# Performance work log

Hardware: AMD Instinct MI355X
Metric: run time of the kernel (lower is better)

Reference implementation:

```python
import jax, jax.numpy as jnp
import numpy as np

D_MODEL = 1024
D_STATE = 512
SEQ_LEN = 16384
R_MIN, R_MAX, MAX_PHASE = 0.0, 1.0, 6.28


def setup_inputs() -> dict:
    key = jax.random.key(0)
    ks = jax.random.split(key, 8)
    inputs = jax.random.normal(ks[0], (SEQ_LEN, D_MODEL), dtype=jnp.float32)
    # parameter init exactly as in the module
    u_nu = jax.random.uniform(ks[1], (D_STATE,), dtype=jnp.float32)
    nu_log = jnp.log(-0.5 * jnp.log(u_nu * (R_MAX ** 2 - R_MIN ** 2) + R_MIN ** 2))
    u_th = jax.random.uniform(ks[2], (D_STATE,), dtype=jnp.float32)
    theta_log = jnp.log(MAX_PHASE * u_th)
    diag_lambda = jnp.exp(-jnp.exp(nu_log) + 1j * jnp.exp(theta_log))
    gamma_log = jnp.log(jnp.sqrt(1.0 - jnp.abs(diag_lambda) ** 2))
    bn = jnp.sqrt(jnp.asarray(2 * D_MODEL, jnp.float32))
    cn = jnp.sqrt(jnp.asarray(D_STATE, jnp.float32))
    B_re = jax.random.normal(ks[3], (D_STATE, D_MODEL), dtype=jnp.float32) / bn
    B_im = jax.random.normal(ks[4], (D_STATE, D_MODEL), dtype=jnp.float32) / bn
    C_re = jax.random.normal(ks[5], (D_MODEL, D_STATE), dtype=jnp.float32) / cn
    C_im = jax.random.normal(ks[6], (D_MODEL, D_STATE), dtype=jnp.float32) / cn
    D = jax.random.normal(ks[7], (D_MODEL,), dtype=jnp.float32)
    return {"inputs": inputs, "nu_log": nu_log, "theta_log": theta_log,
            "gamma_log": gamma_log, "B_re": B_re, "B_im": B_im,
            "C_re": C_re, "C_im": C_im, "D": D}


def _binop(q_i, q_j):
    # associative combine for diagonal linear recurrence h' = a*h + b
    a_i, b_i = q_i
    a_j, b_j = q_j
    return (a_j * a_i, a_j * b_i + b_j)


def reference(inputs, nu_log, theta_log, gamma_log, B_re, B_im, C_re, C_im, D):
    L = inputs.shape[0]
    diag_lambda = jnp.exp(-jnp.exp(nu_log) + 1j * jnp.exp(theta_log))  # (d_state,)
    B_norm = (B_re + 1j * B_im) * jnp.exp(gamma_log)[:, None]          # (d_state, d_model)
    C = C_re + 1j * C_im                                               # (d_model, d_state)
    # Bu[t] = B_norm @ x_t  -> (L, d_state) complex
    Bu = inputs.astype(B_norm.dtype) @ B_norm.T
    Lambda_elems = jnp.broadcast_to(diag_lambda, (L, diag_lambda.shape[0]))
    _, h = jax.lax.associative_scan(_binop, (Lambda_elems, Bu))        # (L, d_state)
    # y_t = Re[C h_t] + D * x_t
    return jnp.real(h @ C.T) + D * inputs
```

## Files before the change

### kernel.cpp

```cpp
#include <hip/hip_runtime.h>
#include <math.h>

#define L_SEQ   16384
#define DMODEL  1024
#define NST     512
#define CHUNK   128
#define NCHUNK  (L_SEQ / CHUNK)

typedef float  f32x4 __attribute__((ext_vector_type(4)));
typedef short  s16x8 __attribute__((ext_vector_type(8)));

__device__ __forceinline__ unsigned short f2bf(float f) {
    union { float f; unsigned int u; } v; v.f = f;
    unsigned int r = v.u + 0x7fffu + ((v.u >> 16) & 1u);
    return (unsigned short)(r >> 16);
}
__device__ __forceinline__ unsigned short f2bf_fast(float f) {
    union { float f; unsigned int u; } v; v.f = f;
    return (unsigned short)((v.u + 0x8000u) >> 16);
}
__device__ __forceinline__ float bf2f(unsigned int h16) {
    union { unsigned int u; float f; } v; v.u = h16 << 16; return v.f;
}
__device__ __forceinline__ void mfma16(f32x4& d, s16x8 a, s16x8 b) {
    asm volatile("v_mfma_f32_16x16x32_bf16 %0, %1, %2, %0"
                 : "+v"(d) : "v"(a), "v"(b));
}
__device__ __forceinline__ uint4 pack8(float4 x, float4 y) {
    union { unsigned short u[8]; uint4 v; } t;
    t.u[0] = f2bf_fast(x.x); t.u[1] = f2bf_fast(x.y);
    t.u[2] = f2bf_fast(x.z); t.u[3] = f2bf_fast(x.w);
    t.u[4] = f2bf_fast(y.x); t.u[5] = f2bf_fast(y.y);
    t.u[6] = f2bf_fast(y.z); t.u[7] = f2bf_fast(y.w);
    return t.v;
}
__device__ __forceinline__ void gload16(const unsigned short* g, unsigned short* l) {
    __builtin_amdgcn_global_load_lds(
        (const __attribute__((address_space(1))) unsigned int*)g,
        (__attribute__((address_space(3))) unsigned int*)l,
        16, 0, 0);
}

__global__ void setup_params(const float* __restrict__ nu_log,
                             const float* __restrict__ theta_log,
                             const float* __restrict__ gamma_log,
                             float* __restrict__ lam,
                             float* __restrict__ lamT,
                             float* __restrict__ gam) {
    int s = threadIdx.x;
    if (s >= NST) return;
    float mod = expf(-expf(nu_log[s]));
    float th  = expf(theta_log[s]);
    float ar = mod * cosf(th);
    float ai = mod * sinf(th);
    lam[s] = ar; lam[NST + s] = ai;
    gam[s] = expf(gamma_log[s]);
    float pr = 1.f, pi = 0.f;
    for (int i = 0; i < CHUNK; ++i) {
        float nr = pr * ar - pi * ai;
        float ni = pr * ai + pi * ar;
        pr = nr; pi = ni;
    }
    lamT[s] = pr; lamT[NST + s] = pi;
}

__global__ void pack_w1(const float* __restrict__ Bre, const float* __restrict__ Bim,
                        unsigned short* __restrict__ W1) {
    int idx = blockIdx.x * 256 + threadIdx.x;
    int n = idx >> 10, k = idx & 1023;
    int s = n >> 1;
    float v = (n & 1) ? Bim[s * DMODEL + k] : Bre[s * DMODEL + k];
    W1[idx] = f2bf(v);
}
__global__ void pack_w2(const float* __restrict__ Cre, const float* __restrict__ Cim,
                        unsigned short* __restrict__ W2) {
    int idx = blockIdx.x * 256 + threadIdx.x;
    int n = idx >> 10, k = idx & 1023;
    int s = k >> 1;
    float v = (k & 1) ? -Cim[n * NST + s] : Cre[n * NST + s];
    W2[idx] = f2bf(v);
}

__global__ __launch_bounds__(256)
void conv_x(const float4* __restrict__ X, uint4* __restrict__ Xb) {
    int i = blockIdx.x * 256 + threadIdx.x;
    float4 a = X[2 * i], b = X[2 * i + 1];
    Xb[i] = pack8(a, b);
}

template<int EPI>
__global__ __launch_bounds__(256, 4)
void gemm_bf16(const unsigned short* __restrict__ A, const unsigned short* __restrict__ B,
               void* __restrict__ out, const float* __restrict__ Dv,
               const float* __restrict__ Xf) {
    const int K = 1024, N = 1024;
    __shared__ __align__(16) unsigned short As[128 * 64];
    __shared__ __align__(16) unsigned short Bs[128 * 64];

    const int tid  = threadIdx.x;
    const int lane = tid & 63;
    const int wave = tid >> 6;
    const int wr   = wave >> 1, wc = wave & 1;
    const int fr   = lane & 15;
    const int g4   = lane >> 4;
    const int f7   = fr & 7;

    const int lin   = blockIdx.y * gridDim.x + blockIdx.x;
    const int n_new = (lin & 7) * 128 + (lin >> 3);
    const int bx = n_new & 7, by = n_new >> 3;
    const int m0 = by * 128, n0 = bx * 128;

    const int srow   = tid >> 3;
    const int schunk = (tid & 7) ^ (srow & 7);
    const unsigned short* Asrc = A + (size_t)(m0 + srow) * K + schunk * 8;
    const unsigned short* Bsrc = B + (size_t)(n0 + srow) * K + schunk * 8;

    f32x4 acc[4][4] = {};

    for (int k0 = 0; k0 < K; k0 += 64) {
        __syncthreads();
        #pragma unroll
        for (int ld = 0; ld < 4; ++ld) {
            gload16(Asrc + (size_t)(ld * 32) * K + k0, &As[ld * 2048 + tid * 8]);
            gload16(Bsrc + (size_t)(ld * 32) * K + k0, &Bs[ld * 2048 + tid * 8]);
        }
        __syncthreads();

        #pragma unroll
        for (int h = 0; h < 2; ++h) {
            s16x8 af[4], bfq[4];
            #pragma unroll
            for (int i = 0; i < 4; ++i) {
                const int row = wr * 64 + i * 16 + fr;
                af[i] = *(const s16x8*)&As[row * 64 + (((h * 4 + g4) ^ f7) << 3)];
            }
            #pragma unroll
            for (int j = 0; j < 4; ++j) {
                const int row = wc * 64 + j * 16 + fr;
                bfq[j] = *(const s16x8*)&Bs[row * 64 + (((h * 4 + g4) ^ f7) << 3)];
            }
            #pragma unroll
            for (int i = 0; i < 4; ++i)
                #pragma unroll
                for (int j = 0; j < 4; ++j)
                    mfma16(acc[i][j], af[i], bfq[j]);
        }
    }

    const int crow = g4 * 4;
    const int ccol = fr;
    #pragma unroll
    for (int i = 0; i < 4; ++i) {
        #pragma unroll
        for (int j = 0; j < 4; ++j) {
            const int mbase = m0 + wr * 64 + i * 16 + crow;
            const int n     = n0 + wc * 64 + j * 16 + ccol;
            #pragma unroll
            for (int r = 0; r < 4; ++r) {
                const int m = mbase + r;
                if (EPI) {
                    ((float*)out)[(size_t)m * N + n] =
                        acc[i][j][r] + Dv[n] * Xf[(size_t)m * N + n];
                } else {
                    ((unsigned short*)out)[(size_t)m * N + n] = f2bf(acc[i][j][r]);
                }
            }
        }
    }
}

__global__ __launch_bounds__(128)
void scan_ends(const unsigned int* __restrict__ Bu, const float* __restrict__ lam,
               const float* __restrict__ gam, float* __restrict__ ends) {
    const int s = blockIdx.y * 128 + threadIdx.x;
    const int c = blockIdx.x;
    const float lr = lam[s], li = lam[NST + s], g = gam[s];
    float hr = 0.f, hi = 0.f;
    size_t base = (size_t)c * CHUNK * NST + s;
    #pragma unroll 4
    for (int t = 0; t < CHUNK; ++t) {
        unsigned int v = Bu[base + (size_t)t * NST];
        float br = g * bf2f(v & 0xffffu);
        float bi = g * bf2f(v >> 16);
        float nr = fmaf(lr, hr, fmaf(-li, hi, br));
        float ni = fmaf(lr, hi, fmaf( li, hr, bi));
        hr = nr; hi = ni;
    }
    ends[(size_t)(c * NST + s) * 2]     = hr;
    ends[(size_t)(c * NST + s) * 2 + 1] = hi;
}

__global__ __launch_bounds__(NST)
void scan_carry(const float* __restrict__ ends, const float* __restrict__ lamT,
                float* __restrict__ car) {
    const int s = threadIdx.x;
    const float ar = lamT[s], ai = lamT[NST + s];
    const float2* E = (const float2*)ends;
    float2*       C = (float2*)car;
    float2 bufA[8], bufB[8];
    #pragma unroll
    for (int k = 0; k < 8; ++k) bufA[k] = E[(size_t)k * NST + s];
    float cr = 0.f, ci = 0.f;
    for (int cc = 0; cc < NCHUNK; cc += 16) {
        #pragma unroll
        for (int k = 0; k < 8; ++k)
            bufB[k] = E[(size_t)(cc + 8 + k) * NST + s];
        #pragma unroll
        for (int k = 0; k < 8; ++k) {
            float2 o; o.x = cr; o.y = ci;
            C[(size_t)(cc + k) * NST + s] = o;
            float nr = fmaf(ar, cr, fmaf(-ai, ci, bufA[k].x));
            float ni = fmaf(ar, ci, fmaf( ai, cr, bufA[k].y));
            cr = nr; ci = ni;
        }
        if (cc + 16 < NCHUNK) {
            #pragma unroll
            for (int k = 0; k < 8; ++k)
                bufA[k] = E[(size_t)(cc + 16 + k) * NST + s];
        }
        #pragma unroll
        for (int k = 0; k < 8; ++k) {
            float2 o; o.x = cr; o.y = ci;
            C[(size_t)(cc + 8 + k) * NST + s] = o;
            float nr = fmaf(ar, cr, fmaf(-ai, ci, bufB[k].x));
            float ni = fmaf(ar, ci, fmaf( ai, cr, bufB[k].y));
            cr = nr; ci = ni;
        }
    }
}

__global__ __launch_bounds__(128)
void scan_h(const unsigned int* __restrict__ Bu, unsigned int* __restrict__ H,
            const float* __restrict__ lam, const float* __restrict__ gam,
            const float* __restrict__ car) {
    const int s = blockIdx.y * 128 + threadIdx.x;
    const int c = blockIdx.x;
    const float lr = lam[s], li = lam[NST + s], g = gam[s];
    float hr = car[(size_t)(c * NST + s) * 2];
    float hi = car[(size_t)(c * NST + s) * 2 + 1];
    size_t base = (size_t)c * CHUNK * NST + s;
    #pragma unroll 4
    for (int t = 0; t < CHUNK; ++t) {
        unsigned int v = Bu[base + (size_t)t * NST];
        float br = g * bf2f(v & 0xffffu);
        float bi = g * bf2f(v >> 16);
        float nr = fmaf(lr, hr, fmaf(-li, hi, br));
        float ni = fmaf(lr, hi, fmaf( li, hr, bi));
        hr = nr; hi = ni;
        H[base + (size_t)t * NST] =
            (unsigned int)f2bf(hr) | ((unsigned int)f2bf(hi) << 16);
    }
}

extern "C" void kernel_launch(void* const* d_in, const int* in_sizes, int n_in,
                              void* d_out, int out_size, void* d_ws, size_t ws_size,
                              hipStream_t stream) {
    const float* X         = (const float*)d_in[0];
    const float* nu_log    = (const float*)d_in[1];
    const float* theta_log = (const float*)d_in[2];
    const float* gamma_log = (const float*)d_in[3];
    const float* Bre       = (const float*)d_in[4];
    const float* Bim       = (const float*)d_in[5];
    const float* Cre       = (const float*)d_in[6];
    const float* Cim       = (const float*)d_in[7];
    const float* Dv        = (const float*)d_in[8];
    float* Y = (float*)d_out;

    char* ws = (char*)d_ws;
    size_t off = 0;
    unsigned short* Xb  = (unsigned short*)(ws + off); off += (size_t)L_SEQ * DMODEL * 2;
    unsigned short* H   = Xb;
    unsigned short* W1  = (unsigned short*)(ws + off); off += (size_t)DMODEL * DMODEL * 2;
    unsigned short* W2  = (unsigned short*)(ws + off); off += (size_t)DMODEL * DMODEL * 2;
    float* lam  = (float*)(ws + off); off += 1024 * 4;
    float* lamT = (float*)(ws + off); off += 1024 * 4;
    float* gam  = (float*)(ws + off); off += 512 * 4;
    float* ends = (float*)(ws + off); off += (size_t)NCHUNK * NST * 2 * 4;
    float* car  = (float*)(ws + off); off += (size_t)NCHUNK * NST * 2 * 4;
    unsigned short* Bu = (unsigned short*)d_out;

    setup_params<<<1, NST, 0, stream>>>(nu_log, theta_log, gamma_log, lam, lamT, gam);
    pack_w1<<<(DMODEL * DMODEL) / 256, 256, 0, stream>>>(Bre, Bim, W1);
    pack_w2<<<(DMODEL * DMODEL) / 256, 256, 0, stream>>>(Cre, Cim, W2);
    conv_x<<<(L_SEQ * DMODEL / 8) / 256, 256, 0, stream>>>((const float4*)X, (uint4*)Xb);

    dim3 gg(8, 128);
    gemm_bf16<0><<<gg, 256, 0, stream>>>(Xb, W1, Bu, nullptr, nullptr);

    dim3 gs(NCHUNK, 4);
    scan_ends<<<gs, 128, 0, stream>>>((const unsigned int*)Bu, lam, gam, ends);
    scan_carry<<<1, NST, 0, stream>>>(ends, lamT, car);
    scan_h<<<gs, 128, 0, stream>>>((const unsigned int*)Bu, (unsigned int*)H, lam, gam, car);

    gemm_bf16<1><<<gg, 256, 0, stream>>>(H, W2, Y, Dv, X);
}
```

Before: 164.4 us.

## Double-buffer GEMM LDS tiles and fuse parameter setup kernels into one launch

The bf16 GEMM now keeps two LDS buffers and issues the global-to-LDS loads for the next K tile before computing the current one. This is meant to hide load latency, and it cuts the barriers per K step from two to one. Occupancy drops, since LDS use doubles and the launch bound minimum goes from four blocks to two. Separately, setup_params, pack_w1 and pack_w2 are merged into one kernel that dispatches on block index, which saves two launches.

```diff
diff --git a/kernel.cpp b/kernel.cpp
--- a/kernel.cpp
+++ b/kernel.cpp
@@ -41,44 +41,46 @@
         16, 0, 0);
 }
 
-__global__ void setup_params(const float* __restrict__ nu_log,
-                             const float* __restrict__ theta_log,
-                             const float* __restrict__ gamma_log,
-                             float* __restrict__ lam,
-                             float* __restrict__ lamT,
-                             float* __restrict__ gam) {
-    int s = threadIdx.x;
-    if (s >= NST) return;
-    float mod = expf(-expf(nu_log[s]));
-    float th  = expf(theta_log[s]);
-    float ar = mod * cosf(th);
-    float ai = mod * sinf(th);
-    lam[s] = ar; lam[NST + s] = ai;
-    gam[s] = expf(gamma_log[s]);
-    float pr = 1.f, pi = 0.f;
-    for (int i = 0; i < CHUNK; ++i) {
-        float nr = pr * ar - pi * ai;
-        float ni = pr * ai + pi * ar;
-        pr = nr; pi = ni;
-    }
-    lamT[s] = pr; lamT[NST + s] = pi;
-}
-
-__global__ void pack_w1(const float* __restrict__ Bre, const float* __restrict__ Bim,
-                        unsigned short* __restrict__ W1) {
-    int idx = blockIdx.x * 256 + threadIdx.x;
-    int n = idx >> 10, k = idx & 1023;
-    int s = n >> 1;
-    float v = (n & 1) ? Bim[s * DMODEL + k] : Bre[s * DMODEL + k];
-    W1[idx] = f2bf(v);
-}
-__global__ void pack_w2(const float* __restrict__ Cre, const float* __restrict__ Cim,
-                        unsigned short* __restrict__ W2) {
-    int idx = blockIdx.x * 256 + threadIdx.x;
-    int n = idx >> 10, k = idx & 1023;
-    int s = k >> 1;
-    float v = (k & 1) ? -Cim[n * NST + s] : Cre[n * NST + s];
-    W2[idx] = f2bf(v);
+__global__ __launch_bounds__(256)
+void setup_all(const float* __restrict__ nu_log, const float* __restrict__ theta_log,
+               const float* __restrict__ gamma_log,
+               const float* __restrict__ Bre, const float* __restrict__ Bim,
+               const float* __restrict__ Cre, const float* __restrict__ Cim,
+               float* __restrict__ lam, float* __restrict__ lamT,
+               float* __restrict__ gam,
+               unsigned short* __restrict__ W1, unsigned short* __restrict__ W2) {
+    const int bid = blockIdx.x;
+    if (bid == 8192) {
+        #pragma unroll
+        for (int q = 0; q < 2; ++q) {
+            int s = threadIdx.x + q * 256;
+            float mod = expf(-expf(nu_log[s]));
+            float th  = expf(theta_log[s]);
+            float ar = mod * cosf(th);
+            float ai = mod * sinf(th);
+            lam[s] = ar; lam[NST + s] = ai;
+            gam[s] = expf(gamma_log[s]);
+            float pr = 1.f, pi = 0.f;
+            for (int i = 0; i < CHUNK; ++i) {
+                float nr = pr * ar - pi * ai;
+                float ni = pr * ai + pi * ar;
+                pr = nr; pi = ni;
+            }
+            lamT[s] = pr; lamT[NST + s] = pi;
+        }
+    } else if (bid < 4096) {
+        int idx = bid * 256 + threadIdx.x;
+        int n = idx >> 10, k = idx & 1023;
+        int s = n >> 1;
+        float v = (n & 1) ? Bim[s * DMODEL + k] : Bre[s * DMODEL + k];
+        W1[idx] = f2bf(v);
+    } else {
+        int idx = (bid - 4096) * 256 + threadIdx.x;
+        int n = idx >> 10, k = idx & 1023;
+        int s = k >> 1;
+        float v = (k & 1) ? -Cim[n * NST + s] : Cre[n * NST + s];
+        W2[idx] = f2bf(v);
+    }
 }
 
 __global__ __launch_bounds__(256)
@@ -88,14 +90,48 @@
     Xb[i] = pack8(a, b);
 }
 
+
+#define STAGE(BUF, T) do {                                                      \
+    const size_t k0_ = (size_t)(T) * 64;                                        \
+    _Pragma("unroll")                                                           \
+    for (int ld = 0; ld < 4; ++ld) {                                            \
+        gload16(Asrc + (size_t)(ld * 32) * 1024 + k0_, &As[BUF][ld * 2048 + tid * 8]); \
+        gload16(Bsrc + (size_t)(ld * 32) * 1024 + k0_, &Bs[BUF][ld * 2048 + tid * 8]); \
+    }                                                                           \
+} while (0)
+
+#define ITER(BUF, T) {                                                          \
+    if ((T) + 1 < 16) STAGE(BUF ^ 1, (T) + 1);                                  \
+    _Pragma("unroll")                                                           \
+    for (int h = 0; h < 2; ++h) {                                               \
+        s16x8 af[4], bfq[4];                                                    \
+        _Pragma("unroll")                                                       \
+        for (int i = 0; i < 4; ++i) {                                           \
+            const int row = wr * 64 + i * 16 + fr;                              \
+            af[i] = *(const s16x8*)&As[BUF][row * 64 + (((h * 4 + g4) ^ f7) << 3)]; \
+        }                                                                       \
+        _Pragma("unroll")                                                       \
+        for (int j = 0; j < 4; ++j) {                                           \
+            const int row = wc * 64 + j * 16 + fr;                              \
+            bfq[j] = *(const s16x8*)&Bs[BUF][row * 64 + (((h * 4 + g4) ^ f7) << 3)]; \
+        }                                                                       \
+        _Pragma("unroll")                                                       \
+        for (int i = 0; i < 4; ++i)                                             \
+            _Pragma("unroll")                                                   \
+            for (int j = 0; j < 4; ++j)                                         \
+                mfma16(acc[i][j], af[i], bfq[j]);                               \
+    }                                                                           \
+    __syncthreads();                                                            \
+}
+
 template<int EPI>
-__global__ __launch_bounds__(256, 4)
+__global__ __launch_bounds__(256, 2)
 void gemm_bf16(const unsigned short* __restrict__ A, const unsigned short* __restrict__ B,
                void* __restrict__ out, const float* __restrict__ Dv,
                const float* __restrict__ Xf) {
     const int K = 1024, N = 1024;
-    __shared__ __align__(16) unsigned short As[128 * 64];
-    __shared__ __align__(16) unsigned short Bs[128 * 64];
+    __shared__ __align__(16) unsigned short As[2][128 * 64];
+    __shared__ __align__(16) unsigned short Bs[2][128 * 64];
 
     const int tid  = threadIdx.x;
     const int lane = tid & 63;
@@ -117,34 +153,12 @@
 
     f32x4 acc[4][4] = {};
 
-    for (int k0 = 0; k0 < K; k0 += 64) {
-        __syncthreads();
-        #pragma unroll
-        for (int ld = 0; ld < 4; ++ld) {
-            gload16(Asrc + (size_t)(ld * 32) * K + k0, &As[ld * 2048 + tid * 8]);
-            gload16(Bsrc + (size_t)(ld * 32) * K + k0, &Bs[ld * 2048 + tid * 8]);
-        }
-        __syncthreads();
-
-        #pragma unroll
-        for (int h = 0; h < 2; ++h) {
-            s16x8 af[4], bfq[4];
-            #pragma unroll
-            for (int i = 0; i < 4; ++i) {
-                const int row = wr * 64 + i * 16 + fr;
-                af[i] = *(const s16x8*)&As[row * 64 + (((h * 4 + g4) ^ f7) << 3)];
-            }
-            #pragma unroll
-            for (int j = 0; j < 4; ++j) {
-                const int row = wc * 64 + j * 16 + fr;
-                bfq[j] = *(const s16x8*)&Bs[row * 64 + (((h * 4 + g4) ^ f7) << 3)];
-            }
-            #pragma unroll
-            for (int i = 0; i < 4; ++i)
-                #pragma unroll
-                for (int j = 0; j < 4; ++j)
-                    mfma16(acc[i][j], af[i], bfq[j]);
-        }
+    STAGE(0, 0);
+    __syncthreads();
+
+    for (int t = 0; t < 16; t += 2) {
+        ITER(0, t)
+        ITER(1, t + 1)
     }
 
     const int crow = g4 * 4;
@@ -279,9 +293,8 @@
     float* car  = (float*)(ws + off); off += (size_t)NCHUNK * NST * 2 * 4;
     unsigned short* Bu = (unsigned short*)d_out;
 
-    setup_params<<<1, NST, 0, stream>>>(nu_log, theta_log, gamma_log, lam, lamT, gam);
-    pack_w1<<<(DMODEL * DMODEL) / 256, 256, 0, stream>>>(Bre, Bim, W1);
-    pack_w2<<<(DMODEL * DMODEL) / 256, 256, 0, stream>>>(Cre, Cim, W2);
+    setup_all<<<8193, 256, 0, stream>>>(nu_log, theta_log, gamma_log,
+                                        Bre, Bim, Cre, Cim, lam, lamT, gam, W1, W2);
     conv_x<<<(L_SEQ * DMODEL / 8) / 256, 256, 0, stream>>>((const float4*)X, (uint4*)Xb);
 
     dim3 gg(8, 128);
```

Result: no change. 166.4 us (+1.2%).
